# Kernel tuning notes

Measured on AMD Instinct MI355X. Metric: run time of the kernel, lower is better.

Reference implementation:

```python
import jax, jax.numpy as jnp
import numpy as np

NEG_SLOPE = 0.2
EPS = 1e-16

N_NODES = 10000
N_EDGES = 80000
F_IN = 128
HID = 300
H1 = 5  # first_heads
H3 = 3  # out_head
N_CLASSES = 40


def gat_conv(x, edge_index, W, att_src, att_dst, bias, heads, out_ch, concat):
    """PyG-style GATConv (v1 attention), eval mode (no dropout).

    x: [N, F_in]; edge_index: [2, E] (row 0 = source, row 1 = target),
    self-loops already included. W: [F_in, heads*out_ch];
    att_src/att_dst: [heads, out_ch].
    """
    N = x.shape[0]
    h = (x @ W).reshape(N, heads, out_ch)            # [N, H, C]
    a_src = jnp.einsum('nhc,hc->nh', h, att_src)     # [N, H]
    a_dst = jnp.einsum('nhc,hc->nh', h, att_dst)     # [N, H]
    src, dst = edge_index[0], edge_index[1]
    e = jax.nn.leaky_relu(a_src[src] + a_dst[dst], NEG_SLOPE)  # [E, H]
    # segment softmax over incoming edges of each target node
    m = jax.ops.segment_max(e, dst, num_segments=N)  # [N, H]
    ex = jnp.exp(e - m[dst])
    s = jax.ops.segment_sum(ex, dst, num_segments=N)
    alpha = ex / (s[dst] + EPS)                      # [E, H]
    msg = h[src] * alpha[:, :, None]                 # [E, H, C]
    out = jax.ops.segment_sum(msg, dst, num_segments=N)  # [N, H, C]
    if concat:
        out = out.reshape(N, heads * out_ch)
    else:
        out = out.mean(axis=1)
    return out + bias


def setup_inputs() -> dict:
    key = jax.random.key(0)
    ks = jax.random.split(key, 12)
    glorot = lambda k, shape: jax.random.normal(k, shape, jnp.float32) * np.sqrt(
        2.0 / (shape[0] + shape[-1]))
    x = jax.random.normal(ks[0], (N_NODES, F_IN), jnp.float32)
    edge_index = jax.random.randint(ks[1], (2, N_EDGES), 0, N_NODES, jnp.int64)
    return {
        'x': x,
        'edge_index': edge_index,
        'W1': glorot(ks[2], (F_IN, H1 * HID)),
        'as1': glorot(ks[3], (H1, HID)),
        'ad1': glorot(ks[4], (H1, HID)),
        'b1': jnp.zeros((H1 * HID,), jnp.float32),
        'W2': glorot(ks[5], (H1 * HID, H1 * HID)),
        'as2': glorot(ks[6], (H1, HID)),
        'ad2': glorot(ks[7], (H1, HID)),
        'b2': jnp.zeros((H1 * HID,), jnp.float32),
        'W3': glorot(ks[8], (H1 * HID, H3 * N_CLASSES)),
        'as3': glorot(ks[9], (H3, N_CLASSES)),
        'ad3': glorot(ks[10], (H3, N_CLASSES)),
        'b3': jnp.zeros((N_CLASSES,), jnp.float32),
    }


def reference(x, edge_index, W1, as1, ad1, b1, W2, as2, ad2, b2, W3, as3, ad3, b3):
    N = x.shape[0]
    # PyG GATConv adds self-loops by default
    loops = jnp.arange(N, dtype=edge_index.dtype)
    ei = jnp.concatenate([edge_index, jnp.stack([loops, loops])], axis=1)
    # dropout layers are identity in eval mode
    h = gat_conv(x, ei, W1, as1, ad1, b1, H1, HID, True)
    h = jax.nn.elu(h)
    h2 = gat_conv(h, ei, W2, as2, ad2, b2, H1, HID, True)
    h = jax.nn.elu(h + h2)
    h = gat_conv(h, ei, W3, as3, ad3, b3, H3, N_CLASSES, False)  # [N, n_cls]
    pooled = h.sum(axis=0, keepdims=True)                        # [1, n_cls]
    return (pooled, jax.nn.log_softmax(pooled, axis=1))
```

## Files before the change

kernel.cpp:

```cpp
#include <hip/hip_runtime.h>
#include <hip/hip_bf16.h>
#include <math.h>

#define NN       10000
#define F_IN     128
#define HID      300
#define H1       5
#define H3       3
#define NCLS     40
#define HC1      (H1*HID)
#define HC3      (H3*NCLS)
#define KPAD     1536
#define LD3      128
#define NEG_SLOPE 0.2f
#define EPSV     1e-16f

typedef __attribute__((ext_vector_type(8))) short bf16x8;
typedef __attribute__((ext_vector_type(8))) unsigned short u16x8;
typedef __attribute__((ext_vector_type(4))) float f32x4;

__device__ inline unsigned short f2bf(float f) {
  unsigned int u = __builtin_bit_cast(unsigned int, f);
  unsigned int r = (u + 0x7FFFu + ((u >> 16) & 1u)) >> 16;
  return (unsigned short)r;
}
__device__ inline float bf2f(unsigned short s) {
  unsigned int u = ((unsigned int)s) << 16;
  return __builtin_bit_cast(float, u);
}

__device__ __forceinline__ void gl2lds16(const unsigned short* g, unsigned short* l) {
  __builtin_amdgcn_global_load_lds(
      (const __attribute__((address_space(1))) unsigned int*)(const void*)g,
      (__attribute__((address_space(3))) unsigned int*)(void*)l, 16, 0, 0);
}

__global__ void k_count(const int* __restrict__ ei, int* __restrict__ counts,
                        int E0, int Etot) {
  int e = blockIdx.x * 256 + threadIdx.x;
  if (e >= Etot) return;
  int dst = (e < E0) ? ei[E0 + e] : (e - E0);
  atomicAdd(&counts[dst], 1);
}

__global__ __launch_bounds__(256) void k_scan(const int* __restrict__ counts,
                                              int* __restrict__ offsets,
                                              int* __restrict__ cursor,
                                              int N, int Etot) {
  __shared__ int sh[256];
  const int CH = 40;
  int t = threadIdx.x;
  int base = t * CH;
  int s = 0;
  for (int i = 0; i < CH; i++) {
    int idx = base + i;
    if (idx < N) s += counts[idx];
  }
  sh[t] = s;
  __syncthreads();
  for (int d = 1; d < 256; d <<= 1) {
    int v = (t >= d) ? sh[t - d] : 0;
    __syncthreads();
    sh[t] += v;
    __syncthreads();
  }
  int run = sh[t] - s;
  for (int i = 0; i < CH; i++) {
    int idx = base + i;
    if (idx < N) {
      offsets[idx] = run;
      cursor[idx] = run;
      run += counts[idx];
    }
  }
  if (t == 0) offsets[N] = Etot;
}

__global__ void k_scatter(const int* __restrict__ ei, int* __restrict__ cursor,
                          int* __restrict__ csr_src, int E0, int Etot) {
  int e = blockIdx.x * 256 + threadIdx.x;
  if (e >= Etot) return;
  int src, dst;
  if (e < E0) { src = ei[e]; dst = ei[E0 + e]; }
  else        { src = dst = e - E0; }
  int pos = atomicAdd(&cursor[dst], 1);
  csr_src[pos] = src;
}

__global__ void k_cvt(const float* __restrict__ in, unsigned short* __restrict__ out,
                      int R, int C, int Cpad) {
  long long idx = (long long)blockIdx.x * 256 + threadIdx.x;
  if (idx >= (long long)R * Cpad) return;
  int r = (int)(idx / Cpad), c = (int)(idx - (long long)r * Cpad);
  out[idx] = (c < C) ? f2bf(in[(size_t)r * C + c]) : 0;
}

__global__ __launch_bounds__(256) void k_cvtT(const float* __restrict__ in,
                                              unsigned short* __restrict__ out,
                                              int K, int Nmat, int Kpad) {
  __shared__ float tile[64][65];
  int kt = blockIdx.y * 64, nt = blockIdx.x * 64;
  int c = threadIdx.x & 63, r = threadIdx.x >> 6;
  for (int rr = r; rr < 64; rr += 4) {
    int k = kt + rr, n = nt + c;
    tile[rr][c] = (k < K && n < Nmat) ? in[(size_t)k * Nmat + n] : 0.f;
  }
  __syncthreads();
  for (int rr = r; rr < 64; rr += 4) {
    int n = nt + rr, k = kt + c;
    if (n < Nmat && k < Kpad) out[(size_t)n * Kpad + k] = f2bf(tile[c][rr]);
  }
}

#define BM 128
#define BN 128
#define BK 64

__global__ __launch_bounds__(256) void gemm_mfma(
    const unsigned short* __restrict__ A,
    const unsigned short* __restrict__ Bt,
    unsigned short* __restrict__ Cbf,
    int M, int Kpad, int Nmat, int ldc) {
  __shared__ unsigned short As[BM * BK];
  __shared__ unsigned short Bs[BN * BK];
  int tid = threadIdx.x;
  int lane = tid & 63, wid = tid >> 6;
  int wm = wid >> 1, wn = wid & 1;
  int bm = blockIdx.x * BM, bn = blockIdx.y * BN;
  int quad = lane >> 4, l16 = lane & 15;
  int kq = quad * 8;

  int ar0 = min(bm + (2 * wid) * 16 + l16, M - 1);
  int ar1 = min(bm + (2 * wid + 1) * 16 + l16, M - 1);
  int br0 = min(bn + (2 * wid) * 16 + l16, Nmat - 1);
  int br1 = min(bn + (2 * wid + 1) * 16 + l16, Nmat - 1);
  const unsigned short* gA0 = A + (size_t)ar0 * Kpad + kq;
  const unsigned short* gA1 = A + (size_t)ar1 * Kpad + kq;
  const unsigned short* gB0 = Bt + (size_t)br0 * Kpad + kq;
  const unsigned short* gB1 = Bt + (size_t)br1 * Kpad + kq;
  unsigned short* lA = As + 4 * wid * 512;
  unsigned short* lB = Bs + 4 * wid * 512;

  f32x4 acc[4][4] = {};

  for (int kt = 0; kt < Kpad; kt += BK) {
    gl2lds16(gA0 + kt,      lA);
    gl2lds16(gA0 + kt + 32, lA + 512);
    gl2lds16(gA1 + kt,      lA + 1024);
    gl2lds16(gA1 + kt + 32, lA + 1536);
    gl2lds16(gB0 + kt,      lB);
    gl2lds16(gB0 + kt + 32, lB + 512);
    gl2lds16(gB1 + kt,      lB + 1024);
    gl2lds16(gB1 + kt + 32, lB + 1536);
    __syncthreads();
#pragma unroll
    for (int kh = 0; kh < 2; kh++) {
      bf16x8 af[4], bfr[4];
#pragma unroll
      for (int i = 0; i < 4; i++) {
        af[i]  = *(const bf16x8*)(As + ((wm * 4 + i) * 2 + kh) * 512 + lane * 8);
        bfr[i] = *(const bf16x8*)(Bs + ((wn * 4 + i) * 2 + kh) * 512 + lane * 8);
      }
#pragma unroll
      for (int i = 0; i < 4; i++)
#pragma unroll
        for (int j = 0; j < 4; j++)
          acc[i][j] = __builtin_amdgcn_mfma_f32_16x16x32_bf16(af[i], bfr[j], acc[i][j], 0, 0, 0);
    }
    __syncthreads();
  }

#pragma unroll
  for (int i = 0; i < 4; i++) {
    int rowb = bm + wm * 64 + i * 16 + quad * 4;
#pragma unroll
    for (int j = 0; j < 4; j++) {
      int col = bn + wn * 64 + j * 16 + l16;
      if (col < ldc) {
        bool live = col < Nmat;
#pragma unroll
        for (int r = 0; r < 4; r++) {
          int row = rowb + r;
          if (row < M) Cbf[(size_t)row * ldc + col] = live ? f2bf(acc[i][j][r]) : 0;
        }
      }
    }
  }
}

__global__ __launch_bounds__(64) void k_att(const unsigned short* __restrict__ hfeat,
                                            int ldh,
                                            const float* __restrict__ att_s,
                                            const float* __restrict__ att_d,
                                            float* __restrict__ asrc,
                                            float* __restrict__ adst,
                                            int H, int C) {
  int n = blockIdx.x;
  int t = threadIdx.x;
  const unsigned short* hr = hfeat + (size_t)n * ldh;
  for (int h = 0; h < H; h++) {
    float ps = 0.f, pd = 0.f;
    for (int c = t; c < C; c += 64) {
      float v = bf2f(hr[h * C + c]);
      ps += v * att_s[h * C + c];
      pd += v * att_d[h * C + c];
    }
    for (int o = 32; o > 0; o >>= 1) {
      ps += __shfl_down(ps, o);
      pd += __shfl_down(pd, o);
    }
    if (t == 0) {
      asrc[n * H + h] = ps;
      adst[n * H + h] = pd;
    }
  }
}

__global__ void k_stats(const float* __restrict__ asrc,
                        const float* __restrict__ adst,
                        const int* __restrict__ csr_src,
                        const int* __restrict__ offsets,
                        float* __restrict__ alpha, int N, int H) {
  int t = blockIdx.x * 256 + threadIdx.x;
  if (t >= N * H) return;
  int n = t / H, h = t - n * H;
  int s0 = offsets[n], s1 = offsets[n + 1];
  float ad = adst[t];
  float m = -1e30f;
  for (int p = s0; p < s1; p++) {
    float v = asrc[csr_src[p] * H + h] + ad;
    v = v > 0.f ? v : NEG_SLOPE * v;
    m = fmaxf(m, v);
  }
  float sum = 0.f;
  for (int p = s0; p < s1; p++) {
    float v = asrc[csr_src[p] * H + h] + ad;
    v = v > 0.f ? v : NEG_SLOPE * v;
    float ex = expf(v - m);
    alpha[p * H + h] = ex;
    sum += ex;
  }
  float r = 1.f / (sum + EPSV);
  for (int p = s0; p < s1; p++) alpha[p * H + h] *= r;
}

__global__ void k_agg(const unsigned short* __restrict__ hfeat, int ldh,
                      const float* __restrict__ alpha,
                      const int* __restrict__ csr_src,
                      const int* __restrict__ offsets,
                      const float* __restrict__ bias,
                      const float* __restrict__ prev,
                      float* __restrict__ out_f32,
                      unsigned short* __restrict__ out_bf,
                      const float* __restrict__ b3,
                      float* __restrict__ h3,
                      int HCv, int C, int H, int mode) {
  int n = blockIdx.x;
  int t = threadIdx.x;
  int nthr = blockDim.x;
  int s0 = offsets[n], s1 = offsets[n + 1];
  int col0 = t * 8;
  bool active = col0 < ldh;

  int hj[8];
  if (active) {
#pragma unroll
    for (int j = 0; j < 8; j++) hj[j] = (col0 + j) / C;
  }
  float acc[8] = {};

  __shared__ int s_src[64];
  __shared__ float s_alpha[64 * 8];
  __shared__ float s_out[LD3];

  for (int base = s0; base < s1; base += 64) {
    int chunk = min(64, s1 - base);
    if (t < chunk) s_src[t] = csr_src[base + t];
    for (int i = t; i < chunk * 8; i += nthr) {
      int e = i >> 3, h = i & 7;
      s_alpha[i] = (h < H) ? alpha[(size_t)(base + e) * H + h] : 0.f;
    }
    __syncthreads();
    if (active) {
      u16x8 rv = *(const u16x8*)(hfeat + (size_t)s_src[0] * ldh + col0);
      for (int e = 0; e < chunk; e++) {
        u16x8 cur = rv;
        if (e + 1 < chunk)
          rv = *(const u16x8*)(hfeat + (size_t)s_src[e + 1] * ldh + col0);
        const float* al = s_alpha + e * 8;
#pragma unroll
        for (int j = 0; j < 8; j++) acc[j] += al[hj[j]] * bf2f(cur[j]);
      }
    }
    __syncthreads();
  }

  if (mode == 2) {
    if (active) {
#pragma unroll
      for (int j = 0; j < 8; j++) s_out[col0 + j] = acc[j];
    }
    __syncthreads();
    if (t < NCLS)
      h3[(size_t)n * NCLS + t] =
          (s_out[t] + s_out[NCLS + t] + s_out[2 * NCLS + t]) * (1.f / 3.f) + b3[t];
    return;
  }

  if (!active) return;
#pragma unroll
  for (int j = 0; j < 8; j++) {
    int col = col0 + j;
    float v = 0.f;
    if (col < HCv) {
      v = acc[j] + bias[col];
      if (mode == 1) v += prev[(size_t)n * HCv + col];
      v = v > 0.f ? v : (expf(v) - 1.f);
      if (out_f32) out_f32[(size_t)n * HCv + col] = v;
    }
    out_bf[(size_t)n * ldh + col] = (col < HCv) ? f2bf(v) : 0;
  }
}

__global__ void k_pool(const float* __restrict__ h3, float* __restrict__ pooled,
                       int N) {
  int col = threadIdx.x;
  if (col >= NCLS) return;
  int row = blockIdx.x * 4 + threadIdx.y;
  int stride = gridDim.x * 4;
  float acc = 0.f;
  for (int r = row; r < N; r += stride) acc += h3[(size_t)r * NCLS + col];
  atomicAdd(&pooled[col], acc);
}

__global__ __launch_bounds__(64) void k_final(const float* __restrict__ pooled,
                                              float* __restrict__ out) {
  int t = threadIdx.x;
  float v = (t < NCLS) ? pooled[t] : -INFINITY;
  float m = v;
  for (int o = 32; o > 0; o >>= 1) m = fmaxf(m, __shfl_xor(m, o));
  float ex = (t < NCLS) ? expf(v - m) : 0.f;
  float s = ex;
  for (int o = 32; o > 0; o >>= 1) s += __shfl_xor(s, o);
  float lse = m + logf(s);
  if (t < NCLS) {
    out[t] = v;
    out[NCLS + t] = v - lse;
  }
}

extern "C" void kernel_launch(void* const* d_in, const int* in_sizes, int n_in,
                              void* d_out, int out_size, void* d_ws, size_t ws_size,
                              hipStream_t stream) {
  const float* x   = (const float*)d_in[0];
  const int*   ei  = (const int*)d_in[1];
  const float* W1  = (const float*)d_in[2];
  const float* as1 = (const float*)d_in[3];
  const float* ad1 = (const float*)d_in[4];
  const float* b1  = (const float*)d_in[5];
  const float* W2  = (const float*)d_in[6];
  const float* as2 = (const float*)d_in[7];
  const float* ad2 = (const float*)d_in[8];
  const float* b2  = (const float*)d_in[9];
  const float* W3  = (const float*)d_in[10];
  const float* as3 = (const float*)d_in[11];
  const float* ad3 = (const float*)d_in[12];
  const float* b3  = (const float*)d_in[13];
  float* out = (float*)d_out;

  const int N = NN;
  const int E0 = in_sizes[1] / 2;
  const int Etot = E0 + N;

  float* f = (float*)d_ws;
  float* hbuf1  = f;
  float* asrc   = f + (size_t)N * HC1;
  float* adst   = asrc + (size_t)N * H1;
  float* alphab = adst + (size_t)N * H1;
  float* pooled = alphab + (size_t)Etot * H1;
  float* h3     = pooled + 64;
  int* counts  = (int*)(h3 + (size_t)N * NCLS);
  int* offsets = counts + N;
  int* cursor  = offsets + N + 1;
  int* csr_src = cursor + N;
  uintptr_t pp = (uintptr_t)(csr_src + Etot);
  pp = (pp + 15) & ~(uintptr_t)15;
  unsigned short* hfbf = (unsigned short*)pp;
  unsigned short* abf  = hfbf + (size_t)N * KPAD;
  unsigned short* btbf = abf + (size_t)N * KPAD;

  hipMemsetAsync(counts, 0, (size_t)N * sizeof(int), stream);
  hipMemsetAsync(pooled, 0, 64 * sizeof(float), stream);

  k_count<<<(Etot + 255) / 256, 256, 0, stream>>>(ei, counts, E0, Etot);
  k_scan<<<1, 256, 0, stream>>>(counts, offsets, cursor, N, Etot);
  k_scatter<<<(Etot + 255) / 256, 256, 0, stream>>>(ei, cursor, csr_src, E0, Etot);

  {
    k_cvt<<<((long long)N * F_IN + 255) / 256, 256, 0, stream>>>(x, abf, N, F_IN, F_IN);
    dim3 tg((HC1 + 63) / 64, (F_IN + 63) / 64);
    k_cvtT<<<tg, 256, 0, stream>>>(W1, btbf, F_IN, HC1, F_IN);
    dim3 grid((N + BM - 1) / BM, (HC1 + BN - 1) / BN);
    gemm_mfma<<<grid, 256, 0, stream>>>(abf, btbf, hfbf, N, F_IN, HC1, KPAD);
    k_att<<<N, 64, 0, stream>>>(hfbf, KPAD, as1, ad1, asrc, adst, H1, HID);
    k_stats<<<(N * H1 + 255) / 256, 256, 0, stream>>>(asrc, adst, csr_src, offsets,
                                                      alphab, N, H1);
    k_agg<<<N, 192, 0, stream>>>(hfbf, KPAD, alphab, csr_src, offsets, b1, nullptr,
                                 hbuf1, abf, nullptr, nullptr, HC1, HID, H1, 0);
  }

  {
    dim3 tg((HC1 + 63) / 64, (KPAD + 63) / 64);
    k_cvtT<<<tg, 256, 0, stream>>>(W2, btbf, HC1, HC1, KPAD);
    dim3 grid((N + BM - 1) / BM, (HC1 + BN - 1) / BN);
    gemm_mfma<<<grid, 256, 0, stream>>>(abf, btbf, hfbf, N, KPAD, HC1, KPAD);
    k_att<<<N, 64, 0, stream>>>(hfbf, KPAD, as2, ad2, asrc, adst, H1, HID);
    k_stats<<<(N * H1 + 255) / 256, 256, 0, stream>>>(asrc, adst, csr_src, offsets,
                                                      alphab, N, H1);
    k_agg<<<N, 192, 0, stream>>>(hfbf, KPAD, alphab, csr_src, offsets, b2, hbuf1,
                                 nullptr, abf, nullptr, nullptr, HC1, HID, H1, 1);
  }

  {
    dim3 tg((HC3 + 63) / 64, (KPAD + 63) / 64);
    k_cvtT<<<tg, 256, 0, stream>>>(W3, btbf, HC1, HC3, KPAD);
    dim3 grid((N + BM - 1) / BM, (HC3 + BN - 1) / BN);
    gemm_mfma<<<grid, 256, 0, stream>>>(abf, btbf, hfbf, N, KPAD, HC3, LD3);
    k_att<<<N, 64, 0, stream>>>(hfbf, LD3, as3, ad3, asrc, adst, H3, NCLS);
    k_stats<<<(N * H3 + 255) / 256, 256, 0, stream>>>(asrc, adst, csr_src, offsets,
                                                      alphab, N, H3);
    k_agg<<<N, 64, 0, stream>>>(hfbf, LD3, alphab, csr_src, offsets, nullptr, nullptr,
                                nullptr, nullptr, b3, h3, HC3, NCLS, H3, 2);
  }

  k_pool<<<64, dim3(64, 4), 0, stream>>>(h3, pooled, N);
  k_final<<<1, 64, 0, stream>>>(pooled, out);
}
```

Measured before the change: 627.6 us.

## Fuse attention logits into GEMM epilogue with per-head padded column layout

Removes the separate k_att kernel. The GEMM epilogue now reduces its accumulators against att_src and att_dst and atomically adds the per-row, per-head logits, with memsets re-zeroing the buffers between layers. Head columns are padded to 8-aligned strides (304 and 48) so each 8-wide vector in aggregation belongs to a single head, which cuts the per-element head lookups. The alpha stride is fixed at 8, and the GEMM grid is swapped so column tiles vary fastest. The cost is float atomics, with nondeterministic summation order, plus slightly more padded GEMM columns.

```diff
diff --git a/kernel.cpp b/kernel.cpp
--- a/kernel.cpp
+++ b/kernel.cpp
@@ -9,9 +9,12 @@
 #define H3       3
 #define NCLS     40
 #define HC1      (H1*HID)
-#define HC3      (H3*NCLS)
 #define KPAD     1536
-#define LD3      128
+#define HS12     304
+#define NL12     1520
+#define HS3      48
+#define NL3      144
+#define LD3      160
 #define NEG_SLOPE 0.2f
 #define EPSV     1e-16f
 
@@ -97,18 +100,27 @@
 
 __global__ __launch_bounds__(256) void k_cvtT(const float* __restrict__ in,
                                               unsigned short* __restrict__ out,
-                                              int K, int Nmat, int Kpad) {
+                                              int K, int Nm, int kC, int kS, int Kp,
+                                              int nC, int nS, int Nmp) {
   __shared__ float tile[64][65];
-  int kt = blockIdx.y * 64, nt = blockIdx.x * 64;
+  int k0 = blockIdx.y * 64, n0 = blockIdx.x * 64;
   int c = threadIdx.x & 63, r = threadIdx.x >> 6;
   for (int rr = r; rr < 64; rr += 4) {
-    int k = kt + rr, n = nt + c;
-    tile[rr][c] = (k < K && n < Nmat) ? in[(size_t)k * Nmat + n] : 0.f;
+    int kp = k0 + rr;
+    int np = n0 + c;
+    float v = 0.f;
+    if (kp < Kp && np < Nmp) {
+      int ck = kp % kS, bk = kp / kS;
+      int cn = np % nS, bn_ = np / nS;
+      int ko = bk * kC + ck, no = bn_ * nC + cn;
+      if (ck < kC && ko < K && cn < nC && no < Nm) v = in[(size_t)ko * Nm + no];
+    }
+    tile[rr][c] = v;
   }
   __syncthreads();
   for (int rr = r; rr < 64; rr += 4) {
-    int n = nt + rr, k = kt + c;
-    if (n < Nmat && k < Kpad) out[(size_t)n * Kpad + k] = f2bf(tile[c][rr]);
+    int np = n0 + rr, kp = k0 + c;
+    if (np < Nmp && kp < Kp) out[(size_t)np * Kp + kp] = f2bf(tile[c][rr]);
   }
 }
 
@@ -120,15 +132,19 @@
     const unsigned short* __restrict__ A,
     const unsigned short* __restrict__ Bt,
     unsigned short* __restrict__ Cbf,
-    int M, int Kpad, int Nmat, int ldc) {
+    int M, int Kpad, int Nmat, int ldc,
+    const float* __restrict__ att_s, const float* __restrict__ att_d,
+    float* __restrict__ asrc, float* __restrict__ adst,
+    int H, int HS, int attCH) {
   __shared__ unsigned short As[BM * BK];
   __shared__ unsigned short Bs[BN * BK];
   int tid = threadIdx.x;
   int lane = tid & 63, wid = tid >> 6;
   int wm = wid >> 1, wn = wid & 1;
-  int bm = blockIdx.x * BM, bn = blockIdx.y * BN;
+  int bm = blockIdx.y * BM, bn = blockIdx.x * BN;
   int quad = lane >> 4, l16 = lane & 15;
   int kq = quad * 8;
+  int padper = HS - attCH / H;
 
   int ar0 = min(bm + (2 * wid) * 16 + l16, M - 1);
   int ar1 = min(bm + (2 * wid + 1) * 16 + l16, M - 1);
@@ -186,32 +202,49 @@
       }
     }
   }
-}
-
-__global__ __launch_bounds__(64) void k_att(const unsigned short* __restrict__ hfeat,
-                                            int ldh,
-                                            const float* __restrict__ att_s,
-                                            const float* __restrict__ att_d,
-                                            float* __restrict__ asrc,
-                                            float* __restrict__ adst,
-                                            int H, int C) {
-  int n = blockIdx.x;
-  int t = threadIdx.x;
-  const unsigned short* hr = hfeat + (size_t)n * ldh;
-  for (int h = 0; h < H; h++) {
-    float ps = 0.f, pd = 0.f;
-    for (int c = t; c < C; c += 64) {
-      float v = bf2f(hr[h * C + c]);
-      ps += v * att_s[h * C + c];
-      pd += v * att_d[h * C + c];
-    }
-    for (int o = 32; o > 0; o >>= 1) {
-      ps += __shfl_down(ps, o);
-      pd += __shfl_down(pd, o);
-    }
-    if (t == 0) {
-      asrc[n * H + h] = ps;
-      adst[n * H + h] = pd;
+
+  float as_j[4], ad_j[4];
+  int hj_[4];
+  int colw = bn + wn * 64;
+#pragma unroll
+  for (int j = 0; j < 4; j++) {
+    int colg = colw + j * 16;
+    int h = colg / HS;
+    hj_[j] = h;
+    int col = colg + l16;
+    int idx = col - padper * h;
+    bool ok = (col < Nmat) && (idx < attCH) && (idx >= 0);
+    idx = min(max(idx, 0), attCH - 1);
+    as_j[j] = ok ? att_s[idx] : 0.f;
+    ad_j[j] = ok ? att_d[idx] : 0.f;
+  }
+  int h0 = hj_[0], hlast = hj_[3];
+#pragma unroll
+  for (int i = 0; i < 4; i++) {
+#pragma unroll
+    for (int r = 0; r < 4; r++) {
+      float s0 = 0.f, s1 = 0.f, d0 = 0.f, d1 = 0.f;
+#pragma unroll
+      for (int j = 0; j < 4; j++) {
+        float v = acc[i][j][r];
+        if (hj_[j] == h0) { s0 += v * as_j[j]; d0 += v * ad_j[j]; }
+        else              { s1 += v * as_j[j]; d1 += v * ad_j[j]; }
+      }
+      for (int o = 8; o > 0; o >>= 1) {
+        s0 += __shfl_xor(s0, o); d0 += __shfl_xor(d0, o);
+        s1 += __shfl_xor(s1, o); d1 += __shfl_xor(d1, o);
+      }
+      int row = bm + wm * 64 + i * 16 + quad * 4 + r;
+      if (l16 == 0 && row < M) {
+        if (h0 < H) {
+          atomicAdd(&asrc[(size_t)row * H + h0], s0);
+          atomicAdd(&adst[(size_t)row * H + h0], d0);
+        }
+        if (hlast != h0 && hlast < H) {
+          atomicAdd(&asrc[(size_t)row * H + hlast], s1);
+          atomicAdd(&adst[(size_t)row * H + hlast], d1);
+        }
+      }
     }
   }
 }
@@ -237,11 +270,11 @@
     float v = asrc[csr_src[p] * H + h] + ad;
     v = v > 0.f ? v : NEG_SLOPE * v;
     float ex = expf(v - m);
-    alpha[p * H + h] = ex;
+    alpha[(size_t)p * 8 + h] = ex;
     sum += ex;
   }
   float r = 1.f / (sum + EPSV);
-  for (int p = s0; p < s1; p++) alpha[p * H + h] *= r;
+  for (int p = s0; p < s1; p++) alpha[(size_t)p * 8 + h] *= r;
 }
 
 __global__ void k_agg(const unsigned short* __restrict__ hfeat, int ldh,
@@ -254,19 +287,15 @@
                       unsigned short* __restrict__ out_bf,
                       const float* __restrict__ b3,
                       float* __restrict__ h3,
-                      int HCv, int C, int H, int mode) {
+                      int HS, int C, int H, int mode) {
   int n = blockIdx.x;
   int t = threadIdx.x;
   int nthr = blockDim.x;
   int s0 = offsets[n], s1 = offsets[n + 1];
   int col0 = t * 8;
   bool active = col0 < ldh;
-
-  int hj[8];
-  if (active) {
-#pragma unroll
-    for (int j = 0; j < 8; j++) hj[j] = (col0 + j) / C;
-  }
+  int hj = active ? (col0 / HS) : 0;
+  int cbase = col0 - hj * HS;
   float acc[8] = {};
 
   __shared__ int s_src[64];
@@ -278,7 +307,7 @@
     if (t < chunk) s_src[t] = csr_src[base + t];
     for (int i = t; i < chunk * 8; i += nthr) {
       int e = i >> 3, h = i & 7;
-      s_alpha[i] = (h < H) ? alpha[(size_t)(base + e) * H + h] : 0.f;
+      s_alpha[i] = (h < H) ? alpha[(size_t)(base + e) * 8 + h] : 0.f;
     }
     __syncthreads();
     if (active) {
@@ -287,9 +316,9 @@
         u16x8 cur = rv;
         if (e + 1 < chunk)
           rv = *(const u16x8*)(hfeat + (size_t)s_src[e + 1] * ldh + col0);
-        const float* al = s_alpha + e * 8;
-#pragma unroll
-        for (int j = 0; j < 8; j++) acc[j] += al[hj[j]] * bf2f(cur[j]);
+        float al = s_alpha[e * 8 + hj];
+#pragma unroll
+        for (int j = 0; j < 8; j++) acc[j] += al * bf2f(cur[j]);
       }
     }
     __syncthreads();
@@ -303,22 +332,24 @@
     __syncthreads();
     if (t < NCLS)
       h3[(size_t)n * NCLS + t] =
-          (s_out[t] + s_out[NCLS + t] + s_out[2 * NCLS + t]) * (1.f / 3.f) + b3[t];
+          (s_out[t] + s_out[HS + t] + s_out[2 * HS + t]) * (1.f / 3.f) + b3[t];
     return;
   }
 
   if (!active) return;
 #pragma unroll
   for (int j = 0; j < 8; j++) {
-    int col = col0 + j;
+    int cin = cbase + j;
+    bool live = (hj < H) && (cin < C);
     float v = 0.f;
-    if (col < HCv) {
-      v = acc[j] + bias[col];
-      if (mode == 1) v += prev[(size_t)n * HCv + col];
+    if (live) {
+      int orig = hj * C + cin;
+      v = acc[j] + bias[orig];
+      if (mode == 1) v += prev[(size_t)n * (H * C) + orig];
       v = v > 0.f ? v : (expf(v) - 1.f);
-      if (out_f32) out_f32[(size_t)n * HCv + col] = v;
-    }
-    out_bf[(size_t)n * ldh + col] = (col < HCv) ? f2bf(v) : 0;
+      if (out_f32) out_f32[(size_t)n * (H * C) + orig] = v;
+    }
+    out_bf[(size_t)n * ldh + col0 + j] = live ? f2bf(v) : 0;
   }
 }
 
@@ -377,7 +408,7 @@
   float* asrc   = f + (size_t)N * HC1;
   float* adst   = asrc + (size_t)N * H1;
   float* alphab = adst + (size_t)N * H1;
-  float* pooled = alphab + (size_t)Etot * H1;
+  float* pooled = alphab + (size_t)Etot * 8;
   float* h3     = pooled + 64;
   int* counts  = (int*)(h3 + (size_t)N * NCLS);
   int* offsets = counts + N;
@@ -391,6 +422,7 @@
 
   hipMemsetAsync(counts, 0, (size_t)N * sizeof(int), stream);
   hipMemsetAsync(pooled, 0, 64 * sizeof(float), stream);
+  hipMemsetAsync(asrc, 0, (size_t)2 * N * H1 * sizeof(float), stream);
 
   k_count<<<(Etot + 255) / 256, 256, 0, stream>>>(ei, counts, E0, Etot);
   k_scan<<<1, 256, 0, stream>>>(counts, offsets, cursor, N, Etot);
@@ -398,39 +430,41 @@
 
   {
     k_cvt<<<((long long)N * F_IN + 255) / 256, 256, 0, stream>>>(x, abf, N, F_IN, F_IN);
-    dim3 tg((HC1 + 63) / 64, (F_IN + 63) / 64);
-    k_cvtT<<<tg, 256, 0, stream>>>(W1, btbf, F_IN, HC1, F_IN);
-    dim3 grid((N + BM - 1) / BM, (HC1 + BN - 1) / BN);
-    gemm_mfma<<<grid, 256, 0, stream>>>(abf, btbf, hfbf, N, F_IN, HC1, KPAD);
-    k_att<<<N, 64, 0, stream>>>(hfbf, KPAD, as1, ad1, asrc, adst, H1, HID);
+    dim3 tg((NL12 + 63) / 64, (F_IN + 63) / 64);
+    k_cvtT<<<tg, 256, 0, stream>>>(W1, btbf, F_IN, HC1, F_IN, F_IN, F_IN, HID, HS12, NL12);
+    dim3 grid(KPAD / BN, (N + BM - 1) / BM);
+    gemm_mfma<<<grid, 256, 0, stream>>>(abf, btbf, hfbf, N, F_IN, NL12, KPAD,
+                                        as1, ad1, asrc, adst, H1, HS12, HC1);
     k_stats<<<(N * H1 + 255) / 256, 256, 0, stream>>>(asrc, adst, csr_src, offsets,
                                                       alphab, N, H1);
+    hipMemsetAsync(asrc, 0, (size_t)2 * N * H1 * sizeof(float), stream);
     k_agg<<<N, 192, 0, stream>>>(hfbf, KPAD, alphab, csr_src, offsets, b1, nullptr,
-                                 hbuf1, abf, nullptr, nullptr, HC1, HID, H1, 0);
+                                 hbuf1, abf, nullptr, nullptr, HS12, HID, H1, 0);
   }
 
   {
-    dim3 tg((HC1 + 63) / 64, (KPAD + 63) / 64);
-    k_cvtT<<<tg, 256, 0, stream>>>(W2, btbf, HC1, HC1, KPAD);
-    dim3 grid((N + BM - 1) / BM, (HC1 + BN - 1) / BN);
-    gemm_mfma<<<grid, 256, 0, stream>>>(abf, btbf, hfbf, N, KPAD, HC1, KPAD);
-    k_att<<<N, 64, 0, stream>>>(hfbf, KPAD, as2, ad2, asrc, adst, H1, HID);
+    dim3 tg((NL12 + 63) / 64, KPAD / 64);
+    k_cvtT<<<tg, 256, 0, stream>>>(W2, btbf, HC1, HC1, HID, HS12, KPAD, HID, HS12, NL12);
+    dim3 grid(KPAD / BN, (N + BM - 1) / BM);
+    gemm_mfma<<<grid, 256, 0, stream>>>(abf, btbf, hfbf, N, KPAD, NL12, KPAD,
+                                        as2, ad2, asrc, adst, H1, HS12, HC1);
     k_stats<<<(N * H1 + 255) / 256, 256, 0, stream>>>(asrc, adst, csr_src, offsets,
                                                       alphab, N, H1);
+    hipMemsetAsync(asrc, 0, (size_t)2 * N * H1 * sizeof(float), stream);
     k_agg<<<N, 192, 0, stream>>>(hfbf, KPAD, alphab, csr_src, offsets, b2, hbuf1,
-                                 nullptr, abf, nullptr, nullptr, HC1, HID, H1, 1);
+                                 nullptr, abf, nullptr, nullptr, HS12, HID, H1, 1);
   }
 
   {
-    dim3 tg((HC3 + 63) / 64, (KPAD + 63) / 64);
-    k_cvtT<<<tg, 256, 0, stream>>>(W3, btbf, HC1, HC3, KPAD);
-    dim3 grid((N + BM - 1) / BM, (HC3 + BN - 1) / BN);
-    gemm_mfma<<<grid, 256, 0, stream>>>(abf, btbf, hfbf, N, KPAD, HC3, LD3);
-    k_att<<<N, 64, 0, stream>>>(hfbf, LD3, as3, ad3, asrc, adst, H3, NCLS);
+    dim3 tg((NL3 + 63) / 64, KPAD / 64);
+    k_cvtT<<<tg, 256, 0, stream>>>(W3, btbf, HC1, H3 * NCLS, HID, HS12, KPAD, NCLS, HS3, NL3);
+    dim3 grid((LD3 + BN - 1) / BN, (N + BM - 1) / BM);
+    gemm_mfma<<<grid, 256, 0, stream>>>(abf, btbf, hfbf, N, KPAD, NL3, LD3,
+                                        as3, ad3, asrc, adst, H3, HS3, H3 * NCLS);
     k_stats<<<(N * H3 + 255) / 256, 256, 0, stream>>>(asrc, adst, csr_src, offsets,
                                                       alphab, N, H3);
     k_agg<<<N, 64, 0, stream>>>(hfbf, LD3, alphab, csr_src, offsets, nullptr, nullptr,
-                                nullptr, nullptr, b3, h3, HC3, NCLS, H3, 2);
+                                nullptr, nullptr, b3, h3, HS3, NCLS, H3, 2);
   }
 
   k_pool<<<64, dim3(64, 4), 0, stream>>>(h3, pooled, N);
```

Result: slower. 659.3 us (+5.0%).
